# Kernel tuning notes

Measured on AMD Instinct MI355X. Metric: run time of the kernel, lower is better.

Reference implementation:

```python
import jax, jax.numpy as jnp
import numpy as np

N = 262144  # number of points
W = 256     # feature width


def setup_inputs() -> dict:
    key = jax.random.key(0)
    k1, k2, k3 = jax.random.split(key, 3)
    x = jax.random.normal(k1, (N, W), dtype=jnp.float32)
    # torch nn.Linear(W, 9) layout: weight [out, in], bias [out]
    fc_w = jax.random.normal(k2, (9, W), dtype=jnp.float32) * (1.0 / np.sqrt(W))
    fc_b = jax.random.normal(k3, (9,), dtype=jnp.float32) * 0.01
    return {"x": x, "fc_w": fc_w, "fc_b": fc_b}


def symmetric_orthogonalization(m):
    # m: [n, 3, 3] -> nearest rotation matrix (special orthogonal Procrustes)
    u, s, vt = jnp.linalg.svd(m, full_matrices=False)
    det = jnp.linalg.det(jnp.einsum('nij,njk->nik', u, vt))  # [n]
    ones = jnp.ones_like(det)
    d = jnp.stack([ones, ones, det], axis=-1)  # [n, 3] diag(1, 1, det)
    r = jnp.einsum('nij,nj,njk->nik', u, d, vt)
    return r


def reference(x, fc_w, fc_b):
    # x: [N, W] -> rotations flattened to [N, 9] (out_type='mat', out_rots=1)
    y = x @ fc_w.T + fc_b            # [N, 9]
    m = y.reshape(-1, 3, 3)          # [N, 3, 3]
    r = symmetric_orthogonalization(m)
    return r.reshape(x.shape[:-1] + (9,))
```

## Files before the change

kernel.cpp:

```cpp
#include <hip/hip_runtime.h>
#include <math.h>

#define N_PTS 262144
#define WIDTH 256

__device__ __forceinline__ void jrot(float &app, float &aqq, float &apq,
                                     float &arp, float &arq,
                                     float &vp0, float &vq0,
                                     float &vp1, float &vq1,
                                     float &vp2, float &vq2)
{
    float a = apq;
    if (fabsf(a) < 1e-20f) return;
    float theta = (aqq - app) / (2.0f * a);
    float tt = copysignf(1.0f, theta) / (fabsf(theta) + sqrtf(1.0f + theta * theta));
    float c = 1.0f / sqrtf(1.0f + tt * tt);
    float s = tt * c;
    app -= tt * a;
    aqq += tt * a;
    apq = 0.0f;
    float rp = arp, rq = arq;
    arp = c * rp - s * rq;
    arq = s * rp + c * rq;
    float t0p = vp0, t0q = vq0; vp0 = c * t0p - s * t0q; vq0 = s * t0p + c * t0q;
    float t1p = vp1, t1q = vq1; vp1 = c * t1p - s * t1q; vq1 = s * t1p + c * t1q;
    float t2p = vp2, t2q = vq2; vp2 = c * t2p - s * t2q; vq2 = s * t2p + c * t2q;
}

__global__ __launch_bounds__(256, 4) void so3_kernel(
    const float* __restrict__ x,
    const float* __restrict__ fw,
    const float* __restrict__ fb,
    float* __restrict__ out)
{
    __shared__ float xs[256][33];
    const int t  = threadIdx.x;
    const int p0 = blockIdx.x << 8;

    float y[9];
#pragma unroll
    for (int j = 0; j < 9; ++j) y[j] = 0.f;

    float4 pre[8];
#pragma unroll
    for (int i = 0; i < 8; ++i) {
        const int flat = (i << 8) + t;
        const int row  = flat >> 3;
        const int c4   = flat & 7;
        pre[i] = *reinterpret_cast<const float4*>(
            x + (size_t)(p0 + row) * WIDTH + (c4 << 2));
    }

    for (int kc = 0; kc < 8; ++kc) {
#pragma unroll
        for (int i = 0; i < 8; ++i) {
            const int flat = (i << 8) + t;
            const int row  = flat >> 3;
            const int c    = (flat & 7) << 2;
            xs[row][c + 0] = pre[i].x;
            xs[row][c + 1] = pre[i].y;
            xs[row][c + 2] = pre[i].z;
            xs[row][c + 3] = pre[i].w;
        }
        __syncthreads();

        if (kc < 7) {
            const int k0n = (kc + 1) << 5;
#pragma unroll
            for (int i = 0; i < 8; ++i) {
                const int flat = (i << 8) + t;
                const int row  = flat >> 3;
                const int c4   = flat & 7;
                pre[i] = *reinterpret_cast<const float4*>(
                    x + (size_t)(p0 + row) * WIDTH + k0n + (c4 << 2));
            }
        }

        const int k0 = kc << 5;
#pragma unroll
        for (int kk = 0; kk < 32; ++kk) {
            const float xv = xs[t][kk];
            const int k = k0 + kk;
#pragma unroll
            for (int j = 0; j < 9; ++j)
                y[j] = fmaf(xv, fw[j * WIDTH + k], y[j]);
        }
        __syncthreads();
    }

#pragma unroll
    for (int j = 0; j < 9; ++j) y[j] += fb[j];

    const float m00 = y[0], m01 = y[1], m02 = y[2];
    const float m10 = y[3], m11 = y[4], m12 = y[5];
    const float m20 = y[6], m21 = y[7], m22 = y[8];

    float a00 = m00*m00 + m10*m10 + m20*m20;
    float a01 = m00*m01 + m10*m11 + m20*m21;
    float a02 = m00*m02 + m10*m12 + m20*m22;
    float a11 = m01*m01 + m11*m11 + m21*m21;
    float a12 = m01*m02 + m11*m12 + m21*m22;
    float a22 = m02*m02 + m12*m12 + m22*m22;

    float v[3][3] = { {1,0,0}, {0,1,0}, {0,0,1} };

#pragma unroll
    for (int sw = 0; sw < 5; ++sw) {
        jrot(a00, a11, a01, a02, a12,
             v[0][0], v[0][1], v[1][0], v[1][1], v[2][0], v[2][1]);
        jrot(a00, a22, a02, a01, a12,
             v[0][0], v[0][2], v[1][0], v[1][2], v[2][0], v[2][2]);
        jrot(a11, a22, a12, a01, a02,
             v[0][1], v[0][2], v[1][1], v[1][2], v[2][1], v[2][2]);
    }

    float d0 = a00, d1 = a11, d2 = a22, tmp;
    if (d0 < d1) { tmp=d0; d0=d1; d1=tmp;
        tmp=v[0][0]; v[0][0]=v[0][1]; v[0][1]=tmp;
        tmp=v[1][0]; v[1][0]=v[1][1]; v[1][1]=tmp;
        tmp=v[2][0]; v[2][0]=v[2][1]; v[2][1]=tmp; }
    if (d0 < d2) { tmp=d0; d0=d2; d2=tmp;
        tmp=v[0][0]; v[0][0]=v[0][2]; v[0][2]=tmp;
        tmp=v[1][0]; v[1][0]=v[1][2]; v[1][2]=tmp;
        tmp=v[2][0]; v[2][0]=v[2][2]; v[2][2]=tmp; }
    if (d1 < d2) { tmp=d1; d1=d2; d2=tmp;
        tmp=v[0][1]; v[0][1]=v[0][2]; v[0][2]=tmp;
        tmp=v[1][1]; v[1][1]=v[1][2]; v[1][2]=tmp;
        tmp=v[2][1]; v[2][1]=v[2][2]; v[2][2]=tmp; }

    const float v1x = v[0][0], v1y = v[1][0], v1z = v[2][0];
    const float v2x = v[0][1], v2y = v[1][1], v2z = v[2][1];

    float u1x = m00*v1x + m01*v1y + m02*v1z;
    float u1y = m10*v1x + m11*v1y + m12*v1z;
    float u1z = m20*v1x + m21*v1y + m22*v1z;
    float inv1 = 1.0f / (sqrtf(u1x*u1x + u1y*u1y + u1z*u1z) + 1e-30f);
    u1x *= inv1; u1y *= inv1; u1z *= inv1;

    float u2x = m00*v2x + m01*v2y + m02*v2z;
    float u2y = m10*v2x + m11*v2y + m12*v2z;
    float u2z = m20*v2x + m21*v2y + m22*v2z;
    const float d12 = u1x*u2x + u1y*u2y + u1z*u2z;
    u2x -= d12*u1x; u2y -= d12*u1y; u2z -= d12*u1z;
    float inv2 = 1.0f / (sqrtf(u2x*u2x + u2y*u2y + u2z*u2z) + 1e-30f);
    u2x *= inv2; u2y *= inv2; u2z *= inv2;

    const float u3x = u1y*u2z - u1z*u2y;
    const float u3y = u1z*u2x - u1x*u2z;
    const float u3z = u1x*u2y - u1y*u2x;
    const float v3x = v1y*v2z - v1z*v2y;
    const float v3y = v1z*v2x - v1x*v2z;
    const float v3z = v1x*v2y - v1y*v2x;

    float r[9];
    r[0] = u1x*v1x + u2x*v2x + u3x*v3x;
    r[1] = u1x*v1y + u2x*v2y + u3x*v3y;
    r[2] = u1x*v1z + u2x*v2z + u3x*v3z;
    r[3] = u1y*v1x + u2y*v2x + u3y*v3x;
    r[4] = u1y*v1y + u2y*v2y + u3y*v3y;
    r[5] = u1y*v1z + u2y*v2z + u3y*v3z;
    r[6] = u1z*v1x + u2z*v2x + u3z*v3x;
    r[7] = u1z*v1y + u2z*v2y + u3z*v3y;
    r[8] = u1z*v1z + u2z*v2z + u3z*v3z;

    float* o = out + (size_t)(p0 + t) * 9;
#pragma unroll
    for (int j = 0; j < 9; ++j) o[j] = r[j];
}

extern "C" void kernel_launch(void* const* d_in, const int* in_sizes, int n_in,
                              void* d_out, int out_size, void* d_ws, size_t ws_size,
                              hipStream_t stream) {
    const float* x  = (const float*)d_in[0];
    const float* fw = (const float*)d_in[1];
    const float* fb = (const float*)d_in[2];
    float* out = (float*)d_out;
    dim3 grid(N_PTS / 256), block(256);
    hipLaunchKernelGGL(so3_kernel, grid, block, 0, stream, x, fw, fb, out);
}
```

Measured before the change: 65.81 us.

## Compute linear layer with per-wave row loads and butterfly shuffle reductions

Replaces the LDS-staged per-thread dot product with a wave-per-64-rows scheme. Each lane holds a 4-column slice of the weights in registers, loads one float4 of each row, and reduces the 9 partial sums across the wave with xor shuffles. The lane whose index matches the row keeps that row's result. This drops the shared-memory tiles and block barriers, but adds 54 cross-lane shuffles per row and puts each wave's loads on a serial 64-iteration loop, which may hide memory latency less well.

```diff
diff --git a/kernel.cpp b/kernel.cpp
--- a/kernel.cpp
+++ b/kernel.cpp
@@ -33,63 +33,47 @@
     const float* __restrict__ fb,
     float* __restrict__ out)
 {
-    __shared__ float xs[256][33];
-    const int t  = threadIdx.x;
-    const int p0 = blockIdx.x << 8;
+    const int lane = threadIdx.x & 63;
+    const int wid  = (blockIdx.x << 2) + (threadIdx.x >> 6);
+    const int r0   = wid << 6;
+
+    float4 w[9];
+#pragma unroll
+    for (int j = 0; j < 9; ++j)
+        w[j] = *reinterpret_cast<const float4*>(fw + j * WIDTH + (lane << 2));
+
+    float yk[9];
+#pragma unroll
+    for (int j = 0; j < 9; ++j) yk[j] = 0.f;
+
+    const float* xbase = x + ((size_t)r0 * WIDTH) + (lane << 2);
+
+#pragma unroll 2
+    for (int i = 0; i < 64; ++i) {
+        const float4 v = *reinterpret_cast<const float4*>(xbase + (size_t)i * WIDTH);
+        float p[9];
+#pragma unroll
+        for (int j = 0; j < 9; ++j) {
+            p[j] = v.x * w[j].x;
+            p[j] = fmaf(v.y, w[j].y, p[j]);
+            p[j] = fmaf(v.z, w[j].z, p[j]);
+            p[j] = fmaf(v.w, w[j].w, p[j]);
+        }
+#pragma unroll
+        for (int m = 1; m < 64; m <<= 1) {
+#pragma unroll
+            for (int j = 0; j < 9; ++j)
+                p[j] += __shfl_xor(p[j], m, 64);
+        }
+        if (lane == i) {
+#pragma unroll
+            for (int j = 0; j < 9; ++j) yk[j] = p[j];
+        }
+    }
 
     float y[9];
 #pragma unroll
-    for (int j = 0; j < 9; ++j) y[j] = 0.f;
-
-    float4 pre[8];
-#pragma unroll
-    for (int i = 0; i < 8; ++i) {
-        const int flat = (i << 8) + t;
-        const int row  = flat >> 3;
-        const int c4   = flat & 7;
-        pre[i] = *reinterpret_cast<const float4*>(
-            x + (size_t)(p0 + row) * WIDTH + (c4 << 2));
-    }
-
-    for (int kc = 0; kc < 8; ++kc) {
-#pragma unroll
-        for (int i = 0; i < 8; ++i) {
-            const int flat = (i << 8) + t;
-            const int row  = flat >> 3;
-            const int c    = (flat & 7) << 2;
-            xs[row][c + 0] = pre[i].x;
-            xs[row][c + 1] = pre[i].y;
-            xs[row][c + 2] = pre[i].z;
-            xs[row][c + 3] = pre[i].w;
-        }
-        __syncthreads();
-
-        if (kc < 7) {
-            const int k0n = (kc + 1) << 5;
-#pragma unroll
-            for (int i = 0; i < 8; ++i) {
-                const int flat = (i << 8) + t;
-                const int row  = flat >> 3;
-                const int c4   = flat & 7;
-                pre[i] = *reinterpret_cast<const float4*>(
-                    x + (size_t)(p0 + row) * WIDTH + k0n + (c4 << 2));
-            }
-        }
-
-        const int k0 = kc << 5;
-#pragma unroll
-        for (int kk = 0; kk < 32; ++kk) {
-            const float xv = xs[t][kk];
-            const int k = k0 + kk;
-#pragma unroll
-            for (int j = 0; j < 9; ++j)
-                y[j] = fmaf(xv, fw[j * WIDTH + k], y[j]);
-        }
-        __syncthreads();
-    }
-
-#pragma unroll
-    for (int j = 0; j < 9; ++j) y[j] += fb[j];
+    for (int j = 0; j < 9; ++j) y[j] = yk[j] + fb[j];
 
     const float m00 = y[0], m01 = y[1], m02 = y[2];
     const float m10 = y[3], m11 = y[4], m12 = y[5];
@@ -163,7 +147,7 @@
     r[7] = u1z*v1y + u2z*v2y + u3z*v3y;
     r[8] = u1z*v1z + u2z*v2z + u3z*v3z;
 
-    float* o = out + (size_t)(p0 + t) * 9;
+    float* o = out + (size_t)(r0 + lane) * 9;
 #pragma unroll
     for (int j = 0; j < 9; ++j) o[j] = r[j];
 }
```

Result: slower. 165.6 us (+151.6%).
